# Performance work log

Measured on AMD Instinct MI355X. Metric: run time of the kernel, lower is better.

The kernel has to match this reference:

```python
import jax, jax.numpy as jnp
import numpy as np

B, S, D, H = 4, 2048, 1024, 16
HD = D // H  # head dim = 64


def setup_inputs() -> dict:
    key = jax.random.key(0)
    ks = jax.random.split(key, 10)
    std = 1.0 / np.sqrt(D)
    return {
        "Q": jax.random.normal(ks[0], (B, S, D), jnp.float32),
        "Q_lev": jax.random.normal(ks[1], (B, S, D), jnp.float32),
        "K": jax.random.normal(ks[2], (B, S, D), jnp.float32),
        "K_lev": jax.random.normal(ks[3], (B, S, D), jnp.float32),
        "V": jax.random.normal(ks[4], (B, S, D), jnp.float32),
        "V_lev": jax.random.normal(ks[5], (B, S, D), jnp.float32),
        "Wq": jax.random.normal(ks[6], (D, D), jnp.float32) * std,
        "bq": jnp.zeros((D,), jnp.float32),
        "Wk": jax.random.normal(ks[7], (D, D), jnp.float32) * std,
        "bk": jnp.zeros((D,), jnp.float32),
        "Wv": jax.random.normal(ks[8], (D, D), jnp.float32) * std,
        "bv": jnp.zeros((D,), jnp.float32),
        "Wo": jax.random.normal(ks[9], (D, D), jnp.float32) * std,
        "bo": jnp.zeros((D,), jnp.float32),
    }


def _heads(x):
    # [B,S,D] -> [B,H,S,HD]
    return x.reshape(B, S, H, HD).transpose(0, 2, 1, 3)


def reference(Q, Q_lev, K, K_lev, V, V_lev, Wq, bq, Wk, bk, Wv, bv, Wo, bo):
    q = _heads(Q @ Wq + bq + Q_lev)
    k = _heads(K @ Wk + bk + K_lev)
    v = _heads(V @ Wv + bv + V_lev)
    scores = jnp.einsum("bhqd,bhkd->bhqk", q, k) / np.sqrt(HD).astype(np.float32)
    probs = jax.nn.softmax(scores, axis=-1)  # attn_dropout rate 0 -> identity
    ctx = jnp.einsum("bhqk,bhkd->bhqd", probs, v)
    ctx = ctx.transpose(0, 2, 1, 3).reshape(B, S, D)
    return ctx @ Wo + bo  # proj_dropout rate 0 -> identity
```

## Files before the change

### kernel.cpp

```cpp
#include <hip/hip_runtime.h>
#include <hip/hip_bf16.h>

#define Bq 4
#define Sq 2048
#define Dq 1024
#define Hq 16
#define HDq 64
#define MR (Bq*Sq)

typedef __attribute__((ext_vector_type(8))) short bf16x8;
typedef __attribute__((ext_vector_type(4))) float f32x4;
typedef __attribute__((ext_vector_type(16))) float f32x16;

__device__ __forceinline__ unsigned short f2bf(float f){
  unsigned int x = __builtin_bit_cast(unsigned int, f);
  x += 0x7fffu + ((x >> 16) & 1u);
  return (unsigned short)(x >> 16);
}

__device__ __forceinline__ unsigned cvtpk(float a, float b){
  unsigned r;
  asm("v_cvt_pk_bf16_f32 %0, %1, %2" : "=v"(r) : "v"(a), "v"(b));
  return r;
}

#define MFMA(a,b,c)   __builtin_amdgcn_mfma_f32_16x16x32_bf16((a),(b),(c),0,0,0)
#define MFMA32(a,b,c) __builtin_amdgcn_mfma_f32_32x32x16_bf16((a),(b),(c),0,0,0)

#define SC_Q 0.18033688f

__device__ __forceinline__ void gload16(const unsigned short* g, unsigned short* l){
  __builtin_amdgcn_global_load_lds(
      (const __attribute__((address_space(1))) void*)g,
      (__attribute__((address_space(3))) void*)l, 16, 0, 0);
}

__global__ __launch_bounds__(256) void cvt_bf16x3(
    const float* __restrict__ X0, const float* __restrict__ X1, const float* __restrict__ X2,
    unsigned short* __restrict__ O0, unsigned short* __restrict__ O1, unsigned short* __restrict__ O2)
{
  const int z = blockIdx.y;
  const float* X = z==0?X0 : z==1?X1 : X2;
  unsigned short* O = z==0?O0 : z==1?O1 : O2;
  const size_t i = ((size_t)blockIdx.x*256 + threadIdx.x)*8;
  const float4 a = *(const float4*)(X+i);
  const float4 b = *(const float4*)(X+i+4);
  union { unsigned u[4]; int4 v; } pk;
  pk.u[0] = cvtpk(a.x, a.y);
  pk.u[1] = cvtpk(a.z, a.w);
  pk.u[2] = cvtpk(b.x, b.y);
  pk.u[3] = cvtpk(b.z, b.w);
  *(int4*)(O+i) = pk.v;
}

__global__ __launch_bounds__(256) void transpose_w(
    const float* __restrict__ W0, const float* __restrict__ W1,
    const float* __restrict__ W2, const float* __restrict__ W3,
    unsigned short* __restrict__ T0, unsigned short* __restrict__ T1,
    unsigned short* __restrict__ T2, unsigned short* __restrict__ T3)
{
  __shared__ float tile[32][33];
  const int z = blockIdx.z;
  const float* W = z==0?W0 : z==1?W1 : z==2?W2 : W3;
  unsigned short* T = z==0?T0 : z==1?T1 : z==2?T2 : T3;
  const int k0 = blockIdx.x*32, n0 = blockIdx.y*32;
  const int tx = threadIdx.x & 31, ty = threadIdx.x >> 5;
  #pragma unroll
  for (int i=0;i<4;i++) tile[ty+i*8][tx] = W[(size_t)(k0+ty+i*8)*Dq + n0+tx];
  __syncthreads();
  #pragma unroll
  for (int i=0;i<4;i++) T[(size_t)(n0+ty+i*8)*Dq + k0+tx] = f2bf(tile[tx][ty+i*8]);
}

__global__ __launch_bounds__(256) void transpose_v(
    const unsigned short* __restrict__ Vb, unsigned short* __restrict__ Vo)
{
  __shared__ unsigned short t2[64][72];
  const int bh = blockIdx.y;
  const int b = bh >> 4, h = bh & 15;
  const int s0 = blockIdx.x * 64;
  const int tid = threadIdx.x;
  const int r = tid >> 3, c8 = tid & 7;
  #pragma unroll
  for (int i=0;i<2;i++){
    int s = r + i*32;
    union { int4 v; unsigned short u[8]; } uu;
    uu.v = *(const int4*)(Vb + ((size_t)b*Sq + s0 + s)*Dq + h*HDq + c8*8);
    #pragma unroll
    for (int jj=0;jj<8;jj++){
      int j = (jj + c8) & 7;
      t2[c8*8 + j][s] = uu.u[j];
    }
  }
  __syncthreads();
  #pragma unroll
  for (int i=0;i<2;i++){
    int d = r + i*32;
    *(int4*)(Vo + ((size_t)bh*HDq + d)*Sq + s0 + c8*8) = *(const int4*)&t2[d][c8*8];
  }
}

__device__ __forceinline__ void gemm_loop(const unsigned short* __restrict__ A,
    const unsigned short* __restrict__ Bt,
    int bm, int bn, unsigned short* Al, unsigned short* Bl, f32x4 acc[4][4])
{
  const int tid = threadIdx.x;
  const int lane = tid & 63, wid = tid >> 6;
  const int lr = lane & 15, lg = lane >> 4;
  const int wm = wid >> 1, wn = wid & 1;

  #define STG(buf, k0) { \
    unsigned short* Ad = Al + (buf)*4096 + wid*512; \
    unsigned short* Bd = Bl + (buf)*4096 + wid*512; \
    _Pragma("unroll") \
    for (int i=0;i<2;i++){ \
      const int row = i*64 + (tid>>2); \
      const int cl  = (tid&3) ^ ((row>>1)&3); \
      gload16(A  + (size_t)(bm*128+row)*Dq + (k0) + cl*8, Ad + i*2048); \
      gload16(Bt + (size_t)(bn*128+row)*Dq + (k0) + cl*8, Bd + i*2048); \
    } }

  STG(0, 0);
  STG(1, 32);
  asm volatile("s_waitcnt vmcnt(4)" ::: "memory");
  __syncthreads();

  const int cr = (lg ^ ((lr >> 1) & 3)) * 8;
  for (int t = 0; t < 32; ++t){
    const int buf = t % 3;
    const unsigned short* Ab = Al + buf*4096;
    const unsigned short* Bb = Bl + buf*4096;
    bf16x8 af[4], bfv[4];
    #pragma unroll
    for (int mt=0;mt<4;mt++) af[mt]  = *(const bf16x8*)(Ab + (wm*64+mt*16+lr)*32 + cr);
    #pragma unroll
    for (int nt=0;nt<4;nt++) bfv[nt] = *(const bf16x8*)(Bb + (wn*64+nt*16+lr)*32 + cr);

    if (t + 2 < 32) {
      STG((t+2)%3, (t+2)*32);
      asm volatile("s_waitcnt vmcnt(4)" ::: "memory");
    } else if (t == 30) {
      asm volatile("s_waitcnt vmcnt(0)" ::: "memory");
    }

    #pragma unroll
    for (int mt=0;mt<4;mt++)
      #pragma unroll
      for (int nt=0;nt<4;nt++)
        acc[mt][nt] = MFMA(af[mt], bfv[nt], acc[mt][nt]);

    __syncthreads();
  }
  #undef STG
}

__global__ __launch_bounds__(256, 3) void proj_gemm(
    const unsigned short* __restrict__ Aq, const unsigned short* __restrict__ Ak, const unsigned short* __restrict__ Av,
    const float* __restrict__ Lq, const float* __restrict__ Lk, const float* __restrict__ Lv,
    const unsigned short* __restrict__ Tq, const unsigned short* __restrict__ Tk, const unsigned short* __restrict__ Tv,
    const float* __restrict__ bqp, const float* __restrict__ bkp, const float* __restrict__ bvp,
    unsigned short* __restrict__ Oq, unsigned short* __restrict__ Ok, unsigned short* __restrict__ Ov)
{
  __shared__ __align__(16) unsigned short Al[3*4096];
  __shared__ __align__(16) unsigned short Bl[3*4096];

  const int bid = blockIdx.x;
  const int swz = (bid & 7)*192 + (bid >> 3);
  const int z   = swz >> 9;
  const int rem = swz & 511;
  const int bm  = rem >> 3, bn = rem & 7;

  const unsigned short* A = z==0?Aq : z==1?Ak : Av;
  const float* Lev = z==0?Lq : z==1?Lk : Lv;
  const unsigned short* Bt = z==0?Tq : z==1?Tk : Tv;
  const float* bias = z==0?bqp : z==1?bkp : bvp;
  unsigned short* Out = z==0?Oq : z==1?Ok : Ov;
  const float scl = (z==0) ? SC_Q : 1.0f;

  f32x4 acc[4][4];
  #pragma unroll
  for (int mt=0;mt<4;mt++)
    #pragma unroll
    for (int nt=0;nt<4;nt++) acc[mt][nt] = (f32x4){0.f,0.f,0.f,0.f};

  gemm_loop(A, Bt, bm, bn, Al, Bl, acc);

  const int tid = threadIdx.x, lane = tid&63, wid = tid>>6;
  const int lr = lane&15, lg = lane>>4, wm = wid>>1, wn = wid&1;
  const int colb = bn*128 + wn*64;
  float bcol[4];
  #pragma unroll
  for (int nt=0;nt<4;nt++) bcol[nt] = bias[colb + nt*16 + lr];
  #pragma unroll
  for (int mt=0;mt<4;mt++){
    int g = bm*128 + wm*64 + mt*16 + lg*4;
    #pragma unroll
    for (int r=0;r<4;r++){
      size_t ro = (size_t)(g+r)*Dq;
      #pragma unroll
      for (int nt=0;nt<4;nt++){
        int col = colb + nt*16 + lr;
        float v = (acc[mt][nt][r] + bcol[nt] + Lev[ro + col]) * scl;
        Out[ro + col] = f2bf(v);
      }
    }
  }
}

__device__ __forceinline__ float comb_max(float x){ return fmaxf(x, __shfl_xor(x, 32, 64)); }
__device__ __forceinline__ float comb_sum(float x){ return x + __shfl_xor(x, 32, 64); }
__device__ __forceinline__ float max3(float a, float b, float c){ return fmaxf(fmaxf(a,b),c); }

__device__ __forceinline__ void pack_p(const f32x16& t, int hi, bf16x8& c0, bf16x8& c1){
  unsigned w[8];
  #pragma unroll
  for (int j=0;j<8;j++) w[j] = cvtpk(t[2*j], t[2*j+1]);
  unsigned x[8];
  #pragma unroll
  for (int j=0;j<8;j++) x[j] = (unsigned)__shfl_xor((int)w[j], 32, 64);
  union { unsigned u[4]; bf16x8 v; } p0, p1;
  p0.u[0] = hi ? x[2] : w[0];
  p0.u[1] = hi ? x[3] : w[1];
  p0.u[2] = hi ? w[2] : x[0];
  p0.u[3] = hi ? w[3] : x[1];
  p1.u[0] = hi ? x[6] : w[4];
  p1.u[1] = hi ? x[7] : w[5];
  p1.u[2] = hi ? w[6] : x[4];
  p1.u[3] = hi ? w[7] : x[5];
  c0 = p0.v; c1 = p1.v;
}

__global__ __launch_bounds__(512, 4) void attn_k(
    const unsigned short* qb, const unsigned short* __restrict__ kb,
    const unsigned short* __restrict__ vt, unsigned short* cb)
{
  __shared__ unsigned short Kl[2][64*64];
  __shared__ unsigned short Vl[2][64*64];
  __shared__ float Rl[8][32];

  const int bid = blockIdx.x;
  const int swz = (bid & 7)*64 + (bid >> 3);
  const int qt = swz & 7, bh = swz >> 3;
  const int b = bh >> 4, h = bh & 15;
  const size_t base = (size_t)b*Sq*Dq + (size_t)h*HDq;

  const int tid = threadIdx.x, lane = tid & 63, wid = tid >> 6;
  const int ln31 = lane & 31, hi = lane >> 5;
  const int q0 = qt*256 + wid*32;

  bf16x8 qf[4];
  {
    const unsigned short* qp = qb + base + (size_t)(q0 + ln31)*Dq + hi*8;
    #pragma unroll
    for (int dk=0;dk<4;dk++) qf[dk] = *(const bf16x8*)(qp + dk*16);
  }

  const int kRow = tid >> 3, kCh = tid & 7;
  const unsigned short* kSrc = kb + base + (size_t)kRow*Dq + kCh*8;
  const unsigned short* vSrc = vt + ((size_t)bh*HDq + kRow)*Sq + kCh*8;
  const int wOff = kRow*64 + ((kCh ^ (kRow & 7))*8);

  int4 kreg = *(const int4*)kSrc;
  int4 vreg = *(const int4*)vSrc;
  *(int4*)&Kl[0][wOff] = kreg;
  *(int4*)&Vl[0][wOff] = vreg;

  f32x16 o0 = (f32x16)(0.0f), o1 = (f32x16)(0.0f);
  float m = -1e30f, l = 0.f;

  for (int kt = 0; kt < Sq/64; ++kt){
    __syncthreads();
    const int p = kt & 1;
    if (kt+1 < Sq/64){
      kreg = *(const int4*)(kSrc + (size_t)(kt+1)*64*Dq);
      vreg = *(const int4*)(vSrc + (kt+1)*64);
    }

    f32x16 t0 = (f32x16)(0.0f), t1 = (f32x16)(0.0f);
    __builtin_amdgcn_s_setprio(1);
    #pragma unroll
    for (int dk=0;dk<4;dk++){
      const int c = hi + dk*2;
      bf16x8 kf0 = *(const bf16x8*)&Kl[p][(ln31)*64    + ((c ^ (ln31 & 7))*8)];
      bf16x8 kf1 = *(const bf16x8*)&Kl[p][(32+ln31)*64 + ((c ^ (ln31 & 7))*8)];
      t0 = MFMA32(kf0, qf[dk], t0);
      t1 = MFMA32(kf1, qf[dk], t1);
    }
    __builtin_amdgcn_s_setprio(0);

    float u0 = max3(max3(t0[0], t0[1],  t0[2]),  max3(t0[3],  t0[4],  t0[5]),
                    max3(t0[6], t0[7],  t0[8]));
    float u1 = max3(max3(t0[9], t0[10], t0[11]), max3(t0[12], t0[13], t0[14]),
                    t0[15]);
    float u2 = max3(max3(t1[0], t1[1],  t1[2]),  max3(t1[3],  t1[4],  t1[5]),
                    max3(t1[6], t1[7],  t1[8]));
    float u3 = max3(max3(t1[9], t1[10], t1[11]), max3(t1[12], t1[13], t1[14]),
                    t1[15]);
    float tmax = comb_max(max3(max3(u0, u1, u2), u3, -1e30f));

    if (__any(tmax > m + 8.0f)){
      float mn = fmaxf(m, tmax);
      float al = __builtin_amdgcn_exp2f(m - mn);
      m = mn;
      l *= al;
      if (hi == 0) Rl[wid][ln31] = al;
      asm volatile("" ::: "memory");
      f32x4 av[4];
      #pragma unroll
      for (int g=0; g<4; g++) av[g] = *(const f32x4*)&Rl[wid][g*8 + hi*4];
      #pragma unroll
      for (int r=0;r<16;r++){ o0[r] *= av[r>>2][r&3]; o1[r] *= av[r>>2][r&3]; }
    }

    float s0 = 0.f, s1 = 0.f, s2 = 0.f, s3 = 0.f;
    #pragma unroll
    for (int r=0;r<16;r+=4){
      float a0 = __builtin_amdgcn_exp2f(t0[r]   - m); t0[r]   = a0; s0 += a0;
      float a1 = __builtin_amdgcn_exp2f(t0[r+1] - m); t0[r+1] = a1; s1 += a1;
      float a2 = __builtin_amdgcn_exp2f(t0[r+2] - m); t0[r+2] = a2; s2 += a2;
      float a3 = __builtin_amdgcn_exp2f(t0[r+3] - m); t0[r+3] = a3; s3 += a3;
    }
    #pragma unroll
    for (int r=0;r<16;r+=4){
      float a0 = __builtin_amdgcn_exp2f(t1[r]   - m); t1[r]   = a0; s0 += a0;
      float a1 = __builtin_amdgcn_exp2f(t1[r+1] - m); t1[r+1] = a1; s1 += a1;
      float a2 = __builtin_amdgcn_exp2f(t1[r+2] - m); t1[r+2] = a2; s2 += a2;
      float a3 = __builtin_amdgcn_exp2f(t1[r+3] - m); t1[r+3] = a3; s3 += a3;
    }
    l += comb_sum((s0 + s1) + (s2 + s3));

    bf16x8 pa0, pa1, pa2, pa3;
    pack_p(t0, hi, pa0, pa1);
    pack_p(t1, hi, pa2, pa3);
    __builtin_amdgcn_s_setprio(1);
    #pragma unroll
    for (int c=0;c<4;c++){
      bf16x8 pa = c==0?pa0 : c==1?pa1 : c==2?pa2 : pa3;
      const int vc = 2*c + hi;
      bf16x8 vf0 = *(const bf16x8*)&Vl[p][(ln31)*64    + ((vc ^ (ln31 & 7))*8)];
      bf16x8 vf1 = *(const bf16x8*)&Vl[p][(32+ln31)*64 + ((vc ^ (ln31 & 7))*8)];
      o0 = MFMA32(pa, vf0, o0);
      o1 = MFMA32(pa, vf1, o1);
    }
    __builtin_amdgcn_s_setprio(0);

    if (kt+1 < Sq/64){
      const int pn = p ^ 1;
      *(int4*)&Kl[pn][wOff] = kreg;
      *(int4*)&Vl[pn][wOff] = vreg;
    }
  }

  float linv = __builtin_amdgcn_rcpf(l);
  if (hi == 0) Rl[wid][ln31] = linv;
  asm volatile("" ::: "memory");
  f32x4 lv[4];
  #pragma unroll
  for (int g=0; g<4; g++) lv[g] = *(const f32x4*)&Rl[wid][g*8 + hi*4];
  #pragma unroll
  for (int r=0;r<16;r++){
    int q = (r&3) + 8*(r>>2) + 4*hi;
    size_t ro = base + (size_t)(q0 + q)*Dq;
    cb[ro + ln31]      = f2bf(o0[r] * lv[r>>2][r&3]);
    cb[ro + 32 + ln31] = f2bf(o1[r] * lv[r>>2][r&3]);
  }
}

__global__ __launch_bounds__(256, 3) void out_gemm(
    const unsigned short* __restrict__ Ctx, const unsigned short* __restrict__ To,
    const float* __restrict__ bop, float* __restrict__ Out)
{
  __shared__ __align__(16) unsigned short Al[3*4096];
  __shared__ __align__(16) unsigned short Bl[3*4096];

  const int bid = blockIdx.x;
  const int swz = (bid & 7)*64 + (bid >> 3);
  const int bm  = swz >> 3, bn = swz & 7;

  f32x4 acc[4][4];
  #pragma unroll
  for (int mt=0;mt<4;mt++)
    #pragma unroll
    for (int nt=0;nt<4;nt++) acc[mt][nt] = (f32x4){0.f,0.f,0.f,0.f};

  gemm_loop(Ctx, To, bm, bn, Al, Bl, acc);

  const int tid = threadIdx.x, lane = tid&63, wid = tid>>6;
  const int lr = lane&15, lg = lane>>4, wm = wid>>1, wn = wid&1;
  const int colb = bn*128 + wn*64;
  float bcol[4];
  #pragma unroll
  for (int nt=0;nt<4;nt++) bcol[nt] = bop[colb + nt*16 + lr];
  #pragma unroll
  for (int mt=0;mt<4;mt++){
    int g = bm*128 + wm*64 + mt*16 + lg*4;
    #pragma unroll
    for (int r=0;r<4;r++){
      size_t ro = (size_t)(g+r)*Dq;
      #pragma unroll
      for (int nt=0;nt<4;nt++){
        int col = colb + nt*16 + lr;
        Out[ro + col] = acc[mt][nt][r] + bcol[nt];
      }
    }
  }
}

extern "C" void kernel_launch(void* const* d_in, const int* in_sizes, int n_in,
                              void* d_out, int out_size, void* d_ws, size_t ws_size,
                              hipStream_t stream) {
  const float* Q    = (const float*)d_in[0];
  const float* Qlev = (const float*)d_in[1];
  const float* K    = (const float*)d_in[2];
  const float* Klev = (const float*)d_in[3];
  const float* V    = (const float*)d_in[4];
  const float* Vlev = (const float*)d_in[5];
  const float* Wq   = (const float*)d_in[6];
  const float* bq   = (const float*)d_in[7];
  const float* Wk   = (const float*)d_in[8];
  const float* bk   = (const float*)d_in[9];
  const float* Wv   = (const float*)d_in[10];
  const float* bv   = (const float*)d_in[11];
  const float* Wo   = (const float*)d_in[12];
  const float* bo   = (const float*)d_in[13];

  unsigned short* qbuf = (unsigned short*)d_ws;
  unsigned short* kbuf = qbuf + (size_t)MR*Dq;
  unsigned short* vbuf = kbuf + (size_t)MR*Dq;
  unsigned short* xq   = vbuf + (size_t)MR*Dq;
  unsigned short* xk   = xq   + (size_t)MR*Dq;
  unsigned short* xv   = xk   + (size_t)MR*Dq;
  unsigned short* Tq   = xv   + (size_t)MR*Dq;
  unsigned short* Tk   = Tq + (size_t)Dq*Dq;
  unsigned short* Tv   = Tk + (size_t)Dq*Dq;
  unsigned short* To   = Tv + (size_t)Dq*Dq;
  unsigned short* vtb  = xq;

  cvt_bf16x3<<<dim3(MR*Dq/(256*8), 3), 256, 0, stream>>>(Q, K, V, xq, xk, xv);
  transpose_w<<<dim3(Dq/32, Dq/32, 4), 256, 0, stream>>>(Wq,Wk,Wv,Wo, Tq,Tk,Tv,To);
  proj_gemm<<<dim3(1536), 256, 0, stream>>>(
      xq,xk,xv, Qlev,Klev,Vlev, Tq,Tk,Tv, bq,bk,bv, qbuf,kbuf,vbuf);
  transpose_v<<<dim3(Sq/64, Bq*Hq), 256, 0, stream>>>(vbuf, vtb);
  attn_k<<<dim3(512), 512, 0, stream>>>(qbuf, kbuf, vtb, qbuf);
  out_gemm<<<dim3(512), 256, 0, stream>>>(qbuf, To, bo, (float*)d_out);
}
```

Measured before the change: 248.9 us.

## Software-pipeline QK^T one tile ahead of softmax and PV in attention

The attention loop now computes the QK^T scores for the next key tile while the current tile's softmax and PV MFMAs run. K is prefetched two tiles ahead and V one tile ahead, and the first tile's scores are computed before the loop. This is meant to hide the exp/max VALU work behind MFMA work and keep the matrix unit busy. pack_p also drops from eight cross-half shuffles to four by selecting which words to exchange before the shuffle. The setprio hints are removed, and the extra live accumulators raise register pressure, which may hurt occupancy at 512 threads with 4 blocks per CU.

```diff
diff --git a/kernel.cpp b/kernel.cpp
--- a/kernel.cpp
+++ b/kernel.cpp
@@ -215,18 +215,23 @@
   unsigned w[8];
   #pragma unroll
   for (int j=0;j<8;j++) w[j] = cvtpk(t[2*j], t[2*j+1]);
-  unsigned x[8];
-  #pragma unroll
-  for (int j=0;j<8;j++) x[j] = (unsigned)__shfl_xor((int)w[j], 32, 64);
+  unsigned z0 = hi ? w[0] : w[2];
+  unsigned z1 = hi ? w[1] : w[3];
+  unsigned z2 = hi ? w[4] : w[6];
+  unsigned z3 = hi ? w[5] : w[7];
+  unsigned x0 = (unsigned)__shfl_xor((int)z0, 32, 64);
+  unsigned x1 = (unsigned)__shfl_xor((int)z1, 32, 64);
+  unsigned x2 = (unsigned)__shfl_xor((int)z2, 32, 64);
+  unsigned x3 = (unsigned)__shfl_xor((int)z3, 32, 64);
   union { unsigned u[4]; bf16x8 v; } p0, p1;
-  p0.u[0] = hi ? x[2] : w[0];
-  p0.u[1] = hi ? x[3] : w[1];
-  p0.u[2] = hi ? w[2] : x[0];
-  p0.u[3] = hi ? w[3] : x[1];
-  p1.u[0] = hi ? x[6] : w[4];
-  p1.u[1] = hi ? x[7] : w[5];
-  p1.u[2] = hi ? w[6] : x[4];
-  p1.u[3] = hi ? w[7] : x[5];
+  p0.u[0] = hi ? x0   : w[0];
+  p0.u[1] = hi ? x1   : w[1];
+  p0.u[2] = hi ? w[2] : x0;
+  p0.u[3] = hi ? w[3] : x1;
+  p1.u[0] = hi ? x2   : w[4];
+  p1.u[1] = hi ? x3   : w[5];
+  p1.u[2] = hi ? w[6] : x2;
+  p1.u[3] = hi ? w[7] : x3;
   c0 = p0.v; c1 = p1.v;
 }
 
@@ -260,42 +265,56 @@
   const unsigned short* vSrc = vt + ((size_t)bh*HDq + kRow)*Sq + kCh*8;
   const int wOff = kRow*64 + ((kCh ^ (kRow & 7))*8);
 
-  int4 kreg = *(const int4*)kSrc;
-  int4 vreg = *(const int4*)vSrc;
-  *(int4*)&Kl[0][wOff] = kreg;
-  *(int4*)&Vl[0][wOff] = vreg;
+  {
+    int4 k0r = *(const int4*)kSrc;
+    int4 v0r = *(const int4*)vSrc;
+    int4 k1r = *(const int4*)(kSrc + (size_t)64*Dq);
+    *(int4*)&Kl[0][wOff] = k0r;
+    *(int4*)&Vl[0][wOff] = v0r;
+    *(int4*)&Kl[1][wOff] = k1r;
+  }
 
   f32x16 o0 = (f32x16)(0.0f), o1 = (f32x16)(0.0f);
   float m = -1e30f, l = 0.f;
 
+  __syncthreads();
+
+  f32x16 c0 = (f32x16)(0.0f), c1 = (f32x16)(0.0f);
+  #pragma unroll
+  for (int dk=0;dk<4;dk++){
+    const int c = hi + dk*2;
+    bf16x8 kf0 = *(const bf16x8*)&Kl[0][(ln31)*64    + ((c ^ (ln31 & 7))*8)];
+    bf16x8 kf1 = *(const bf16x8*)&Kl[0][(32+ln31)*64 + ((c ^ (ln31 & 7))*8)];
+    c0 = MFMA32(kf0, qf[dk], c0);
+    c1 = MFMA32(kf1, qf[dk], c1);
+  }
+
+  int4 kreg = {0,0,0,0}, vreg = {0,0,0,0};
+
   for (int kt = 0; kt < Sq/64; ++kt){
     __syncthreads();
-    const int p = kt & 1;
+    const int pn = (kt+1) & 1;
+    if (kt+2 < Sq/64) kreg = *(const int4*)(kSrc + (size_t)(kt+2)*64*Dq);
+    if (kt+1 < Sq/64) vreg = *(const int4*)(vSrc + (kt+1)*64);
+
+    f32x16 n0 = (f32x16)(0.0f);
     if (kt+1 < Sq/64){
-      kreg = *(const int4*)(kSrc + (size_t)(kt+1)*64*Dq);
-      vreg = *(const int4*)(vSrc + (kt+1)*64);
-    }
-
-    f32x16 t0 = (f32x16)(0.0f), t1 = (f32x16)(0.0f);
-    __builtin_amdgcn_s_setprio(1);
-    #pragma unroll
-    for (int dk=0;dk<4;dk++){
-      const int c = hi + dk*2;
-      bf16x8 kf0 = *(const bf16x8*)&Kl[p][(ln31)*64    + ((c ^ (ln31 & 7))*8)];
-      bf16x8 kf1 = *(const bf16x8*)&Kl[p][(32+ln31)*64 + ((c ^ (ln31 & 7))*8)];
-      t0 = MFMA32(kf0, qf[dk], t0);
-      t1 = MFMA32(kf1, qf[dk], t1);
-    }
-    __builtin_amdgcn_s_setprio(0);
-
-    float u0 = max3(max3(t0[0], t0[1],  t0[2]),  max3(t0[3],  t0[4],  t0[5]),
-                    max3(t0[6], t0[7],  t0[8]));
-    float u1 = max3(max3(t0[9], t0[10], t0[11]), max3(t0[12], t0[13], t0[14]),
-                    t0[15]);
-    float u2 = max3(max3(t1[0], t1[1],  t1[2]),  max3(t1[3],  t1[4],  t1[5]),
-                    max3(t1[6], t1[7],  t1[8]));
-    float u3 = max3(max3(t1[9], t1[10], t1[11]), max3(t1[12], t1[13], t1[14]),
-                    t1[15]);
+      #pragma unroll
+      for (int dk=0;dk<4;dk++){
+        const int c = hi + dk*2;
+        bf16x8 kf0 = *(const bf16x8*)&Kl[pn][(ln31)*64 + ((c ^ (ln31 & 7))*8)];
+        n0 = MFMA32(kf0, qf[dk], n0);
+      }
+    }
+
+    float u0 = max3(max3(c0[0], c0[1],  c0[2]),  max3(c0[3],  c0[4],  c0[5]),
+                    max3(c0[6], c0[7],  c0[8]));
+    float u1 = max3(max3(c0[9], c0[10], c0[11]), max3(c0[12], c0[13], c0[14]),
+                    c0[15]);
+    float u2 = max3(max3(c1[0], c1[1],  c1[2]),  max3(c1[3],  c1[4],  c1[5]),
+                    max3(c1[6], c1[7],  c1[8]));
+    float u3 = max3(max3(c1[9], c1[10], c1[11]), max3(c1[12], c1[13], c1[14]),
+                    c1[15]);
     float tmax = comb_max(max3(max3(u0, u1, u2), u3, -1e30f));
 
     if (__any(tmax > m + 8.0f)){
@@ -315,40 +334,50 @@
     float s0 = 0.f, s1 = 0.f, s2 = 0.f, s3 = 0.f;
     #pragma unroll
     for (int r=0;r<16;r+=4){
-      float a0 = __builtin_amdgcn_exp2f(t0[r]   - m); t0[r]   = a0; s0 += a0;
-      float a1 = __builtin_amdgcn_exp2f(t0[r+1] - m); t0[r+1] = a1; s1 += a1;
-      float a2 = __builtin_amdgcn_exp2f(t0[r+2] - m); t0[r+2] = a2; s2 += a2;
-      float a3 = __builtin_amdgcn_exp2f(t0[r+3] - m); t0[r+3] = a3; s3 += a3;
+      float a0 = __builtin_amdgcn_exp2f(c0[r]   - m); c0[r]   = a0; s0 += a0;
+      float a1 = __builtin_amdgcn_exp2f(c0[r+1] - m); c0[r+1] = a1; s1 += a1;
+      float a2 = __builtin_amdgcn_exp2f(c0[r+2] - m); c0[r+2] = a2; s2 += a2;
+      float a3 = __builtin_amdgcn_exp2f(c0[r+3] - m); c0[r+3] = a3; s3 += a3;
     }
     #pragma unroll
     for (int r=0;r<16;r+=4){
-      float a0 = __builtin_amdgcn_exp2f(t1[r]   - m); t1[r]   = a0; s0 += a0;
-      float a1 = __builtin_amdgcn_exp2f(t1[r+1] - m); t1[r+1] = a1; s1 += a1;
-      float a2 = __builtin_amdgcn_exp2f(t1[r+2] - m); t1[r+2] = a2; s2 += a2;
-      float a3 = __builtin_amdgcn_exp2f(t1[r+3] - m); t1[r+3] = a3; s3 += a3;
+      float a0 = __builtin_amdgcn_exp2f(c1[r]   - m); c1[r]   = a0; s0 += a0;
+      float a1 = __builtin_amdgcn_exp2f(c1[r+1] - m); c1[r+1] = a1; s1 += a1;
+      float a2 = __builtin_amdgcn_exp2f(c1[r+2] - m); c1[r+2] = a2; s2 += a2;
+      float a3 = __builtin_amdgcn_exp2f(c1[r+3] - m); c1[r+3] = a3; s3 += a3;
     }
     l += comb_sum((s0 + s1) + (s2 + s3));
 
-    bf16x8 pa0, pa1, pa2, pa3;
-    pack_p(t0, hi, pa0, pa1);
-    pack_p(t1, hi, pa2, pa3);
-    __builtin_amdgcn_s_setprio(1);
-    #pragma unroll
-    for (int c=0;c<4;c++){
-      bf16x8 pa = c==0?pa0 : c==1?pa1 : c==2?pa2 : pa3;
-      const int vc = 2*c + hi;
-      bf16x8 vf0 = *(const bf16x8*)&Vl[p][(ln31)*64    + ((vc ^ (ln31 & 7))*8)];
-      bf16x8 vf1 = *(const bf16x8*)&Vl[p][(32+ln31)*64 + ((vc ^ (ln31 & 7))*8)];
-      o0 = MFMA32(pa, vf0, o0);
-      o1 = MFMA32(pa, vf1, o1);
-    }
-    __builtin_amdgcn_s_setprio(0);
-
+    {
+      const int p = kt & 1;
+      bf16x8 pa0, pa1, pa2, pa3;
+      pack_p(c0, hi, pa0, pa1);
+      pack_p(c1, hi, pa2, pa3);
+      #pragma unroll
+      for (int c=0;c<4;c++){
+        bf16x8 pa = c==0?pa0 : c==1?pa1 : c==2?pa2 : pa3;
+        const int vc = 2*c + hi;
+        bf16x8 vf0 = *(const bf16x8*)&Vl[p][(ln31)*64    + ((vc ^ (ln31 & 7))*8)];
+        bf16x8 vf1 = *(const bf16x8*)&Vl[p][(32+ln31)*64 + ((vc ^ (ln31 & 7))*8)];
+        o0 = MFMA32(pa, vf0, o0);
+        o1 = MFMA32(pa, vf1, o1);
+      }
+    }
+
+    f32x16 n1 = (f32x16)(0.0f);
     if (kt+1 < Sq/64){
-      const int pn = p ^ 1;
-      *(int4*)&Kl[pn][wOff] = kreg;
-      *(int4*)&Vl[pn][wOff] = vreg;
-    }
+      #pragma unroll
+      for (int dk=0;dk<4;dk++){
+        const int c = hi + dk*2;
+        bf16x8 kf1 = *(const bf16x8*)&Kl[pn][(32+ln31)*64 + ((c ^ (ln31 & 7))*8)];
+        n1 = MFMA32(kf1, qf[dk], n1);
+      }
+    }
+
+    if (kt+2 < Sq/64) *(int4*)&Kl[kt & 1][wOff] = kreg;
+    if (kt+1 < Sq/64) *(int4*)&Vl[pn][wOff]     = vreg;
+
+    c0 = n0; c1 = n1;
   }
 
   float linv = __builtin_amdgcn_rcpf(l);
```

New measurement: 308.6 us. 24.0% more time.
